# Optimization experiments

Measured on AMD Instinct MI355X. Metric: run time of the kernel, lower is better.

Reference implementation:

```python
import jax, jax.numpy as jnp
import numpy as np

NUM_NODES = 64
MAX_P = 8          # max parents per node (band width)
HID = 2 * MAX_P    # padded hidden size (per-node true hidden = 2*p)
BATCH = 131072


def _build_graph():
    """Banded lower-triangular DAG: node i>0 has parents max(0,i-8)..i-1; node 0 -> self."""
    A = np.zeros((NUM_NODES, NUM_NODES), np.int32)
    A[0, 0] = 1
    for i in range(1, NUM_NODES):
        A[i, max(0, i - MAX_P):i] = 1
    parent_idx = np.zeros((NUM_NODES, MAX_P), np.int32)
    in_mask = np.zeros((NUM_NODES, MAX_P), np.float32)
    for i in range(NUM_NODES):
        p = np.nonzero(A[i])[0]
        parent_idx[i, :len(p)] = p
        in_mask[i, :len(p)] = 1.0
    n_par = in_mask.sum(axis=1)  # (N,)
    # node i's true hidden width is 2*p_i; mask padded hidden units
    hid_mask = (np.arange(HID)[None, :] < 2 * n_par[:, None]).astype(np.float32)
    return parent_idx, in_mask, hid_mask


def setup_inputs() -> dict:
    key = jax.random.key(0)
    k_x, k_w1, k_b1, k_w2, k_b2 = jax.random.split(key, 5)
    parent_idx, in_mask, hid_mask = _build_graph()

    gt_labels = jax.random.normal(k_x, (BATCH, NUM_NODES), dtype=jnp.float32)

    # Padded per-node weights; zero out padded input columns / hidden rows so the
    # math equals the original ragged per-node Linear(p,2p)-Tanh-Linear(2p,1).
    bound1 = 1.0 / np.sqrt(MAX_P)
    W1 = jax.random.uniform(k_w1, (NUM_NODES, HID, MAX_P), jnp.float32, -bound1, bound1)
    b1 = jax.random.uniform(k_b1, (NUM_NODES, HID), jnp.float32, -bound1, bound1)
    bound2 = 1.0 / np.sqrt(HID)
    W2 = jax.random.uniform(k_w2, (NUM_NODES, HID), jnp.float32, -bound2, bound2)
    b2 = jax.random.uniform(k_b2, (NUM_NODES,), jnp.float32, -bound2, bound2)

    in_m = jnp.asarray(in_mask)       # (N, P)
    hid_m = jnp.asarray(hid_mask)     # (N, H)
    W1 = W1 * in_m[:, None, :] * hid_m[:, :, None]
    b1 = b1 * hid_m
    W2 = W2 * hid_m

    return {
        "gt_labels": gt_labels,
        "W1": W1, "b1": b1, "W2": W2, "b2": b2,
        "parent_idx": jnp.asarray(parent_idx),
    }


def reference(gt_labels, W1, b1, W2, b2, parent_idx):
    # Gather each node's (padded) parent values: (B, N, P)
    x = gt_labels[:, parent_idx]
    # Per-node tiny MLP, batched over nodes: hidden (B, N, H)
    h = jnp.tanh(jnp.einsum('bnp,nhp->bnh', x, W1) + b1)
    mus = (jnp.einsum('bnh,nh->bn', h, W2) + b2)[..., None]   # (B, N, 1)
    logvars = jnp.zeros_like(mus)
    return mus, logvars
```

## Files before the change

### kernel.cpp

```cpp
#include <hip/hip_runtime.h>


#define BATCH   131072
#define NODES   64
#define HID     16
#define MAXP    8
#define TPB     256
#define NBLOCKS 2048
#define TM      32
#define UNITS   16

typedef float v2     __attribute__((ext_vector_type(2)));
typedef float v4     __attribute__((ext_vector_type(4)));
typedef float f32x16 __attribute__((ext_vector_type(16)));
typedef _Float16 h8v __attribute__((ext_vector_type(8)));
typedef unsigned u32x4 __attribute__((ext_vector_type(4)));

__device__ __forceinline__ v2 tanh2(v2 x) {
    v2 x2  = x * x;
    v2 num = x2 * (x2 + 105.f) + 945.f;
    v2 den = x2 * (x2 * 15.f + 420.f) + 945.f;
    v2 r;
    r.x = __builtin_amdgcn_rcpf(den.x);
    r.y = __builtin_amdgcn_rcpf(den.y);
    return x * num * r;
}

__device__ __forceinline__ unsigned pk16(float a, float b) {
    return __builtin_bit_cast(unsigned, __builtin_amdgcn_cvt_pkrtz(a, b));
}

__global__ __launch_bounds__(TPB, 4)
void prior_kernel(const float* __restrict__ gt,
                  const float* __restrict__ W1,
                  const float* __restrict__ b1,
                  const float* __restrict__ W2,
                  const float* __restrict__ b2,
                  const int*   __restrict__ parent_idx,
                  float* __restrict__ out)
{
    const int lane = threadIdx.x & 63;
    const int widx = threadIdx.x >> 6;
    const int q    = blockIdx.x >> 8;
    const int tc   = blockIdx.x & 255;
    const int pair = q * 4 + widx;
    const int n0   = pair * 2, n1 = n0 + 1;
    const int sl   = lane & 31;
    const int half = lane >> 5;

    h8v afrag;
    #pragma unroll
    for (int j = 0; j < 8; ++j) {
        float w = 0.f;
        if (!half) { if (sl < 16)  w = W1[(n0 * HID + sl) * MAXP + j]; }
        else       { if (sl >= 16) w = W1[(n1 * HID + (sl - 16)) * MAXP + j]; }
        afrag[j] = (_Float16)w;
    }

    f32x16 cfrag;
    float  w2f[16];
    #pragma unroll
    for (int r = 0; r < 16; ++r) {
        const int m = (r & 3) + 8 * (r >> 2) + 4 * half;
        cfrag[r] = (m < 16) ? b1[n0 * HID + m] : b1[n1 * HID + (m - 16)];
        w2f[r]   = (m < 16) ? W2[n0 * HID + m] : W2[n1 * HID + (m - 16)];
    }
    v2 w2v[8];
    #pragma unroll
    for (int i = 0; i < 8; ++i) { v2 t = { w2f[2 * i], w2f[2 * i + 1] }; w2v[i] = t; }
    const float b2v0 = b2[n0], b2v1 = b2[n1];

    const int nd = half ? n1 : n0;
    const int cs = parent_idx[nd * MAXP];
    const unsigned rbase   = (unsigned)tc * 512u + (unsigned)sl;
    unsigned       idx     = rbase * 64u + (unsigned)cs;
    const unsigned ISTEP   = (unsigned)TM * 64u;
    const unsigned idxLast = idx + (UNITS - 1) * ISTEP;
    unsigned       om      = rbase * 64u + (unsigned)nd;
    const unsigned LV      = (unsigned)BATCH * 64u;

    v4 r0 = *(const v4*)(gt + idx);
    v4 r1 = *(const v4*)(gt + idx + 4);

    #pragma unroll 1
    for (int t = 0; t < UNITS; ++t) {
        unsigned nidx = idx + ISTEP;
        if (nidx > idxLast) nidx = idxLast;
        v4 rn0 = *(const v4*)(gt + nidx);
        v4 rn1 = *(const v4*)(gt + nidx + 4);
        idx = nidx;

        u32x4 upk = { pk16(r0.x, r0.y), pk16(r0.z, r0.w),
                      pk16(r1.x, r1.y), pk16(r1.z, r1.w) };
        h8v bfrag = __builtin_bit_cast(h8v, upk);

        f32x16 acc = __builtin_amdgcn_mfma_f32_32x32x16_f16(afrag, bfrag, cfrag, 0, 0, 0);

        v2 s0 = { 0.f, 0.f }, s1 = { 0.f, 0.f };
        #pragma unroll
        for (int i = 0; i < 4; ++i) {
            v2 a = { acc[2 * i], acc[2 * i + 1] };
            s0 = __builtin_elementwise_fma(tanh2(a), w2v[i], s0);
        }
        #pragma unroll
        for (int i = 4; i < 8; ++i) {
            v2 a = { acc[2 * i], acc[2 * i + 1] };
            s1 = __builtin_elementwise_fma(tanh2(a), w2v[i], s1);
        }
        float S0 = s0.x + s0.y;  S0 += __shfl_xor(S0, 32, 64);
        float S1 = s1.x + s1.y;  S1 += __shfl_xor(S1, 32, 64);
        const float mu = half ? (S1 + b2v1) : (S0 + b2v0);

        out[om]      = mu;
        out[om + LV] = 0.f;
        om += ISTEP;
        r0 = rn0; r1 = rn1;
    }
}

extern "C" void kernel_launch(void* const* d_in, const int* in_sizes, int n_in,
                              void* d_out, int out_size, void* d_ws, size_t ws_size,
                              hipStream_t stream)
{
    const float* gt  = (const float*)d_in[0];
    const float* W1  = (const float*)d_in[1];
    const float* b1  = (const float*)d_in[2];
    const float* W2  = (const float*)d_in[3];
    const float* b2  = (const float*)d_in[4];
    const int*   pix = (const int*)d_in[5];
    float* out = (float*)d_out;

    prior_kernel<<<NBLOCKS, TPB, 0, stream>>>(gt, W1, b1, W2, b2, pix, out);
}
```

Before: 170.8 us.

## Process two node pairs per wave and stage outputs in LDS for coalesced stores

Each wave now handles two node pairs (four nodes) instead of one, so a block covers 16 consecutive output columns. Results are staged in a double-buffered shared-memory tile and written back as 8-byte vector stores of contiguous columns, replacing scattered 4-byte scalar stores. The block index mapping is also reordered so neighbouring blocks share row chunks, which should improve L2 reuse of the input rows. In exchange it adds a __syncthreads per iteration, more registers per thread, and half as many blocks in total.

```diff
diff --git a/kernel.cpp b/kernel.cpp
--- a/kernel.cpp
+++ b/kernel.cpp
@@ -6,9 +6,11 @@
 #define HID     16
 #define MAXP    8
 #define TPB     256
-#define NBLOCKS 2048
 #define TM      32
 #define UNITS   16
+#define RCROWS  (TM * UNITS)
+#define NRC     (BATCH / RCROWS)
+#define NBLOCKS (NRC * 4)
 
 typedef float v2     __attribute__((ext_vector_type(2)));
 typedef float v4     __attribute__((ext_vector_type(4)));
@@ -39,82 +41,107 @@
                   const int*   __restrict__ parent_idx,
                   float* __restrict__ out)
 {
-    const int lane = threadIdx.x & 63;
-    const int widx = threadIdx.x >> 6;
-    const int q    = blockIdx.x >> 8;
-    const int tc   = blockIdx.x & 255;
-    const int pair = q * 4 + widx;
-    const int n0   = pair * 2, n1 = n0 + 1;
+    const int tid  = threadIdx.x;
+    const int lane = tid & 63;
+    const int widx = tid >> 6;
     const int sl   = lane & 31;
     const int half = lane >> 5;
 
-    h8v afrag;
+    const int c  = blockIdx.x & 7;
+    const int j  = blockIdx.x >> 3;
+    const int rc = c + 8 * (j >> 2);
+    const int g  = j & 3;
+
+    const int P0 = g * 8 + widx * 2;
+
+    h8v    af[2];
+    f32x16 cf[2];
+    v2     w2v[2][8];
+    float  b2s[2];
+    int    cs[2];
     #pragma unroll
-    for (int j = 0; j < 8; ++j) {
-        float w = 0.f;
-        if (!half) { if (sl < 16)  w = W1[(n0 * HID + sl) * MAXP + j]; }
-        else       { if (sl >= 16) w = W1[(n1 * HID + (sl - 16)) * MAXP + j]; }
-        afrag[j] = (_Float16)w;
+    for (int pl = 0; pl < 2; ++pl) {
+        const int P  = P0 + pl;
+        const int n0 = 2 * P, n1 = n0 + 1;
+        #pragma unroll
+        for (int q = 0; q < 8; ++q) {
+            float w = 0.f;
+            if (!half) { if (sl < 16)  w = W1[(n0 * HID + sl) * MAXP + q]; }
+            else       { if (sl >= 16) w = W1[(n1 * HID + (sl - 16)) * MAXP + q]; }
+            af[pl][q] = (_Float16)w;
+        }
+        float w2f[16];
+        #pragma unroll
+        for (int r = 0; r < 16; ++r) {
+            const int m = (r & 3) + 8 * (r >> 2) + 4 * half;
+            cf[pl][r] = (m < 16) ? b1[n0 * HID + m] : b1[n1 * HID + (m - 16)];
+            w2f[r]    = (m < 16) ? W2[n0 * HID + m] : W2[n1 * HID + (m - 16)];
+        }
+        #pragma unroll
+        for (int i = 0; i < 8; ++i) {
+            v2 t = { w2f[2 * i], w2f[2 * i + 1] };
+            w2v[pl][i] = t;
+        }
+        b2s[pl] = b2[2 * P + half];
+        cs[pl]  = parent_idx[(2 * P + half) * MAXP];
     }
 
-    f32x16 cfrag;
-    float  w2f[16];
+    const unsigned row0 = (unsigned)rc * RCROWS;
+    unsigned xi[2], xmax[2];
+    v4 r0[2], r1[2];
     #pragma unroll
-    for (int r = 0; r < 16; ++r) {
-        const int m = (r & 3) + 8 * (r >> 2) + 4 * half;
-        cfrag[r] = (m < 16) ? b1[n0 * HID + m] : b1[n1 * HID + (m - 16)];
-        w2f[r]   = (m < 16) ? W2[n0 * HID + m] : W2[n1 * HID + (m - 16)];
+    for (int pl = 0; pl < 2; ++pl) {
+        xi[pl]   = (row0 + (unsigned)sl) * 64u + (unsigned)cs[pl];
+        xmax[pl] = xi[pl] + (UNITS - 1) * TM * 64u;
+        r0[pl] = *(const v4*)(gt + xi[pl]);
+        r1[pl] = *(const v4*)(gt + xi[pl] + 4);
+        xi[pl] += TM * 64u;
     }
-    v2 w2v[8];
-    #pragma unroll
-    for (int i = 0; i < 8; ++i) { v2 t = { w2f[2 * i], w2f[2 * i + 1] }; w2v[i] = t; }
-    const float b2v0 = b2[n0], b2v1 = b2[n1];
 
-    const int nd = half ? n1 : n0;
-    const int cs = parent_idx[nd * MAXP];
-    const unsigned rbase   = (unsigned)tc * 512u + (unsigned)sl;
-    unsigned       idx     = rbase * 64u + (unsigned)cs;
-    const unsigned ISTEP   = (unsigned)TM * 64u;
-    const unsigned idxLast = idx + (UNITS - 1) * ISTEP;
-    unsigned       om      = rbase * 64u + (unsigned)nd;
-    const unsigned LV      = (unsigned)BATCH * 64u;
-
-    v4 r0 = *(const v4*)(gt + idx);
-    v4 r1 = *(const v4*)(gt + idx + 4);
+    __shared__ __align__(16) float mt[2][TM][18];
+    const unsigned LV = (unsigned)BATCH * 64u;
+    unsigned ob = (row0 + (unsigned)(tid >> 3)) * 64u
+                + (unsigned)(g * 16 + (tid & 7) * 2);
 
     #pragma unroll 1
     for (int t = 0; t < UNITS; ++t) {
-        unsigned nidx = idx + ISTEP;
-        if (nidx > idxLast) nidx = idxLast;
-        v4 rn0 = *(const v4*)(gt + nidx);
-        v4 rn1 = *(const v4*)(gt + nidx + 4);
-        idx = nidx;
+        #pragma unroll
+        for (int pl = 0; pl < 2; ++pl) {
+            u32x4 upk = { pk16(r0[pl].x, r0[pl].y), pk16(r0[pl].z, r0[pl].w),
+                          pk16(r1[pl].x, r1[pl].y), pk16(r1[pl].z, r1[pl].w) };
+            h8v bfrag = __builtin_bit_cast(h8v, upk);
 
-        u32x4 upk = { pk16(r0.x, r0.y), pk16(r0.z, r0.w),
-                      pk16(r1.x, r1.y), pk16(r1.z, r1.w) };
-        h8v bfrag = __builtin_bit_cast(h8v, upk);
+            const unsigned ni = xi[pl] < xmax[pl] ? xi[pl] : xmax[pl];
+            r0[pl] = *(const v4*)(gt + ni);
+            r1[pl] = *(const v4*)(gt + ni + 4);
+            xi[pl] += TM * 64u;
 
-        f32x16 acc = __builtin_amdgcn_mfma_f32_32x32x16_f16(afrag, bfrag, cfrag, 0, 0, 0);
+            f32x16 acc = __builtin_amdgcn_mfma_f32_32x32x16_f16(af[pl], bfrag, cf[pl], 0, 0, 0);
 
-        v2 s0 = { 0.f, 0.f }, s1 = { 0.f, 0.f };
-        #pragma unroll
-        for (int i = 0; i < 4; ++i) {
-            v2 a = { acc[2 * i], acc[2 * i + 1] };
-            s0 = __builtin_elementwise_fma(tanh2(a), w2v[i], s0);
+            v2 s0 = { 0.f, 0.f }, s1 = { 0.f, 0.f };
+            #pragma unroll
+            for (int i = 0; i < 4; ++i) {
+                v2 a = { acc[2 * i], acc[2 * i + 1] };
+                s0 = __builtin_elementwise_fma(tanh2(a), w2v[pl][i], s0);
+            }
+            #pragma unroll
+            for (int i = 4; i < 8; ++i) {
+                v2 a = { acc[2 * i], acc[2 * i + 1] };
+                s1 = __builtin_elementwise_fma(tanh2(a), w2v[pl][i], s1);
+            }
+            float S0 = s0.x + s0.y;  S0 += __shfl_xor(S0, 32, 64);
+            float S1 = s1.x + s1.y;  S1 += __shfl_xor(S1, 32, 64);
+            const float mu = (half ? S1 : S0) + b2s[pl];
+
+            mt[t & 1][sl][4 * widx + 2 * pl + half] = mu;
         }
-        #pragma unroll
-        for (int i = 4; i < 8; ++i) {
-            v2 a = { acc[2 * i], acc[2 * i + 1] };
-            s1 = __builtin_elementwise_fma(tanh2(a), w2v[i], s1);
-        }
-        float S0 = s0.x + s0.y;  S0 += __shfl_xor(S0, 32, 64);
-        float S1 = s1.x + s1.y;  S1 += __shfl_xor(S1, 32, 64);
-        const float mu = half ? (S1 + b2v1) : (S0 + b2v0);
+        __syncthreads();
 
-        out[om]      = mu;
-        out[om + LV] = 0.f;
-        om += ISTEP;
-        r0 = rn0; r1 = rn1;
+        const v2 mv = *(const v2*)&mt[t & 1][tid >> 3][(tid & 7) * 2];
+        *(v2*)(out + ob) = mv;
+        const v2 z = { 0.f, 0.f };
+        *(v2*)(out + ob + LV) = z;
+        ob += TM * 64u;
     }
 }
 
```

Result: slower. 199.6 us (+16.9%).
